# Optimization experiments

Measured on AMD Instinct MI355X. Metric: run time of the kernel, lower is better.

The kernel has to match this reference:

```python
import jax, jax.numpy as jnp
import numpy as np

B, S, HID, H = 8, 128, 256, 4
DH = HID // H
FF = 4 * HID


def setup_inputs() -> dict:
    key = jax.random.key(0)
    ks = jax.random.split(key, 16)
    n = lambda i, shape: jax.random.normal(ks[i], shape, dtype=jnp.float32) * 0.02
    z = lambda shape: jnp.zeros(shape, dtype=jnp.float32)
    return dict(
        x=jax.random.normal(ks[0], (B, S, HID), dtype=jnp.float32),
        attention_mask=jnp.zeros((B, 1, S, S), dtype=jnp.float32),
        Wq=n(1, (HID, HID)), bq=z((HID,)),
        Wk=n(2, (HID, HID)), bk=z((HID,)),
        Wv=n(3, (HID, HID)), bv=z((HID,)),
        order_w=n(4, (2 * DH,)), order_b=z(()),
        dist_w=n(5, (2 * DH,)), dist_b=z(()),
        scalar=jax.random.normal(ks[6], (1,), dtype=jnp.float32),
        AWq=n(7, (HID, HID)), Abq=z((HID,)),
        AWk=n(8, (HID, HID)), Abk=z((HID,)),
        Wd=n(9, (HID, HID)), bd=z((HID,)),
        g1=jnp.ones((HID,), jnp.float32), beta1=z((HID,)),
        W1=n(10, (HID, FF)), b1=z((FF,)),
        W2=n(11, (FF, HID)), b2=z((HID,)),
        g2=jnp.ones((HID,), jnp.float32), beta2=z((HID,)),
    )


def _ln(t, g, b, eps=1e-12):
    m = t.mean(-1, keepdims=True)
    v = ((t - m) ** 2).mean(-1, keepdims=True)
    return (t - m) / jnp.sqrt(v + eps) * g + b


def _heads(t):
    # [B,S,HID] -> [B,H,S,DH]
    return t.reshape(B, S, H, DH).transpose(0, 2, 1, 3)


def reference(x, attention_mask, Wq, bq, Wk, bk, Wv, bv, order_w, order_b,
              dist_w, dist_b, scalar, AWq, Abq, AWk, Abk, Wd, bd,
              g1, beta1, W1, b1, W2, b2, g2, beta2):
    inv = 1.0 / jnp.sqrt(jnp.float32(DH))
    q = x @ Wq + bq
    k = x @ Wk + bk
    v = x @ Wv + bv
    qh, kh, vh = _heads(q), _heads(k), _heads(v)
    scores = jnp.einsum('bhqd,bhkd->bhqk', qh, kh)  # [B,H,S,S]

    # order/distance affines on concat(q_i, k_j): Linear(2*DH,1) decomposes into
    # per-token projections summed via broadcast (same math, no [B,H,S,S,2*DH] tensor)
    pr_order = jax.nn.sigmoid((qh @ order_w[:DH])[..., :, None]
                              + (kh @ order_w[DH:])[..., None, :] + order_b)
    gd_order = jnp.triu(jnp.ones((S, S), jnp.float32), k=1)
    err_order = (jnp.log(pr_order + 1e-24) * gd_order
                 + jnp.log(1.0 - pr_order + 1e-24) * (1.0 - gd_order))

    idx = jnp.arange(S)
    gd_dist = jnp.log(jnp.abs(idx[None, :] - idx[:, None]).astype(jnp.float32) + 1.0)
    pr_dist = ((qh @ dist_w[:DH])[..., :, None]
               + (kh @ dist_w[DH:])[..., None, :] + dist_b)
    err_dist = -jnp.square(gd_dist - pr_dist) * jnp.square(scalar[0]) * 0.5

    rich_scores = scores + err_order + err_dist
    softm = lambda s: jax.nn.softmax(s * inv + attention_mask, axis=-1)
    rich_probs = softm(rich_scores)
    origin_probs = softm(scores)

    # rich/calibrated combine ('fixed'): softmax(origin + 0.5 * rich)
    combined = jax.nn.softmax(origin_probs + 0.5 * rich_probs, axis=-1)

    # two-level attack attention on transformed mixed q/k
    aq, ak = _heads(q @ AWq + Abq), _heads(k @ AWk + Abk)
    attack_probs = softm(jnp.einsum('bhqd,bhkd->bhqk', aq, ak))
    final_probs = jax.nn.softmax(combined + 0.5 * attack_probs, axis=-1)

    ctx = jnp.einsum('bhqk,bhkd->bhqd', final_probs, vh)
    ctx = ctx.transpose(0, 2, 1, 3).reshape(B, S, HID)
    h = _ln(ctx @ Wd + bd + x, g1, beta1)
    f = jax.nn.gelu(h @ W1 + b1, approximate=False) @ W2 + b2
    return _ln(f + h, g2, beta2)
```

## Files before the change

### kernel.cpp

```cpp
#include <hip/hip_runtime.h>
#include <hip/hip_bf16.h>
#include <math.h>

#define B_  8
#define S_  128
#define HID_ 256
#define H_  4
#define DH_ 64
#define FF_ 1024
#define M_  (B_ * S_)

typedef _Float16 half_t;
typedef __attribute__((ext_vector_type(8))) _Float16 half8;
typedef __attribute__((ext_vector_type(4))) float floatx4;

enum { EP_F32 = 0, EP_F16 = 1, EP_F16B = 2, EP_GELU = 3, EP_PROJ = 4 };

__device__ __forceinline__ floatx4 mfma16(half8 a, half8 b, floatx4 c) {
    return __builtin_amdgcn_mfma_f32_16x16x32_f16(a, b, c, 0, 0, 0);
}

__device__ __forceinline__ float wred_sum(float v) {
#pragma unroll
    for (int o = 32; o >= 1; o >>= 1) v += __shfl_xor(v, o, 64);
    return v;
}
__device__ __forceinline__ float block_sum_256(float v, float* s4, int tid) {
    v = wred_sum(v);
    __syncthreads();
    if ((tid & 63) == 0) s4[tid >> 6] = v;
    __syncthreads();
    return s4[0] + s4[1] + s4[2] + s4[3];
}
__device__ __forceinline__ float qred_sum(float v) {
#pragma unroll
    for (int o = 1; o < 16; o <<= 1) v += __shfl_xor(v, o, 64);
    return v;
}
__device__ __forceinline__ void sm8(float (&v)[8]) {
    float s = 0.f;
#pragma unroll
    for (int j = 0; j < 8; ++j) { v[j] = __expf(v[j]); s += v[j]; }
    s = qred_sum(s);
    float r = 1.f / s;
#pragma unroll
    for (int j = 0; j < 8; ++j) v[j] *= r;
}

template<int EPI>
__device__ __forceinline__ void mgemm(
    const half_t* __restrict__ A, int ldA,
    const half_t* __restrict__ Bt, int ldB,
    int kLen, int m0, int n0,
    const float* __restrict__ bias,
    float* __restrict__ Cf, half_t* __restrict__ Ch, int ldC,
    const float* __restrict__ pw1, const float* __restrict__ pw2,
    float* __restrict__ po1, float* __restrict__ po2, int hsel)
{
    __shared__ half8 Asf[2][4][64];
    __shared__ half8 Bsf[2][4][64];

    const int tid = threadIdx.x;
    const int w = tid >> 6, l = tid & 63;
    const int sr = tid >> 2;
    const int sq = tid & 3;
    const int sdst = (sr & 15) | (sq << 4);
    const int smt = sr >> 4;
    const half_t* Ap = A + (size_t)(m0 + sr) * ldA + sq * 8;
    const half_t* Bp = Bt + (size_t)(n0 + sr) * ldB + sq * 8;

    half8 ra, rb;
    auto fetch = [&](int t) {
        ra = *(const half8*)(Ap + t * 32);
        rb = *(const half8*)(Bp + t * 32);
    };
    auto commit = [&](int buf) {
        Asf[buf][smt][sdst] = ra;
        Bsf[buf][smt][sdst] = rb;
    };

    floatx4 zero = {0.f, 0.f, 0.f, 0.f};
    floatx4 acc[4] = {zero, zero, zero, zero};
    const int kt = kLen >> 5;

    fetch(0);
    commit(0);
    __syncthreads();
    for (int t = 0; t < kt; ++t) {
        const bool more = (t + 1 < kt);
        if (more) fetch(t + 1);
        const int buf = t & 1;
        half8 a = Asf[buf][w][l];
        acc[0] = mfma16(a, Bsf[buf][0][l], acc[0]);
        acc[1] = mfma16(a, Bsf[buf][1][l], acc[1]);
        acc[2] = mfma16(a, Bsf[buf][2][l], acc[2]);
        acc[3] = mfma16(a, Bsf[buf][3][l], acc[3]);
        if (more) {
            commit((t + 1) & 1);
            __syncthreads();
        }
    }

    const int quad = l >> 4, lc = l & 15;
    const int rowb = m0 + w * 16 + quad * 4;
    float bvv[4] = {0.f, 0.f, 0.f, 0.f};
    if (EPI >= EP_F16B) {
#pragma unroll
        for (int nt = 0; nt < 4; ++nt) bvv[nt] = bias[n0 + nt * 16 + lc];
    }
    float pw1v[4], pw2v[4];
    if (EPI == EP_PROJ) {
#pragma unroll
        for (int nt = 0; nt < 4; ++nt) {
            pw1v[nt] = pw1[nt * 16 + lc];
            pw2v[nt] = pw2[nt * 16 + lc];
        }
    }
#pragma unroll
    for (int rr = 0; rr < 4; ++rr) {
        float ov[4];
#pragma unroll
        for (int nt = 0; nt < 4; ++nt) {
            float o = acc[nt][rr];
            if (EPI >= EP_F16B) o += bvv[nt];
            if (EPI == EP_GELU) o = 0.5f * o * (1.f + erff(o * 0.70710678118654752f));
            ov[nt] = o;
            const size_t ci = (size_t)(rowb + rr) * ldC + n0 + nt * 16 + lc;
            if (EPI == EP_F32) Cf[ci] = o;
            else Ch[ci] = (half_t)o;
        }
        if (EPI == EP_PROJ) {
            float po = ov[0] * pw1v[0] + ov[1] * pw1v[1] + ov[2] * pw1v[2] + ov[3] * pw1v[3];
            float pd = ov[0] * pw2v[0] + ov[1] * pw2v[1] + ov[2] * pw2v[2] + ov[3] * pw2v[3];
#pragma unroll
            for (int off = 1; off < 16; off <<= 1) {
                po += __shfl_xor(po, off, 64);
                pd += __shfl_xor(pd, off, 64);
            }
            if (lc == 0) {
                const int m = rowb + rr;
                const int idx = ((m >> 7) * H_ + hsel) * S_ + (m & 127);
                po1[idx] = po;
                po2[idx] = pd;
            }
        }
    }
}

__global__ __launch_bounds__(256) void prep_kernel(
    const float* __restrict__ x,
    const float* __restrict__ Wq, const float* __restrict__ Wk,
    const float* __restrict__ Wv, const float* __restrict__ Wd,
    const float* __restrict__ AWq, const float* __restrict__ AWk,
    const float* __restrict__ W1, const float* __restrict__ W2,
    half_t* __restrict__ x16, half_t* __restrict__ Wq16n, half_t* __restrict__ Wk16n,
    half_t* __restrict__ WqT, half_t* __restrict__ WkT, half_t* __restrict__ WvT,
    half_t* __restrict__ WdT, half_t* __restrict__ AWqT, half_t* __restrict__ AWkT,
    half_t* __restrict__ W1T, half_t* __restrict__ W2T)
{
    const int z = blockIdx.z, bx = blockIdx.x, by = blockIdx.y;
    const int tid = threadIdx.x;
    if (z < 3) {
        const float* src = (z == 0) ? x : (z == 1) ? Wq : Wk;
        half_t* dst = (z == 0) ? x16 : (z == 1) ? Wq16n : Wk16n;
        const int total = (z == 0) ? M_ * HID_ : HID_ * HID_;
        const int bid = by * 16 + bx;
        if (bid * 1024 < total) {
            const int base = bid * 1024 + tid * 4;
            float4 vv = *(const float4*)(src + base);
            dst[base + 0] = (half_t)vv.x;
            dst[base + 1] = (half_t)vv.y;
            dst[base + 2] = (half_t)vv.z;
            dst[base + 3] = (half_t)vv.w;
        }
        return;
    }
    const float* src; half_t* dst; int K, N, k0, n0;
    if (z <= 8) {
        const float* ins[6] = {Wq, Wk, Wv, Wd, AWq, AWk};
        half_t* outs[6] = {WqT, WkT, WvT, WdT, AWqT, AWkT};
        src = ins[z - 3]; dst = outs[z - 3];
        K = 256; N = 256; k0 = bx * 64; n0 = by * 64;
        if (bx >= 4 || by >= 4) return;
    } else if (z == 9) {
        src = W1; dst = W1T; K = 256; N = 1024;
        k0 = bx * 64; n0 = by * 64;
        if (bx >= 4) return;
    } else {
        src = W2; dst = W2T; K = 1024; N = 256;
        k0 = by * 64; n0 = bx * 64;
        if (bx >= 4) return;
    }
    __shared__ half_t tl[64][72];
    const int r = tid >> 2, c0 = (tid & 3) * 16;
#pragma unroll 4
    for (int i = 0; i < 16; ++i)
        tl[c0 + i][r] = (half_t)src[(size_t)(k0 + r) * N + n0 + c0 + i];
    __syncthreads();
#pragma unroll 4
    for (int i = 0; i < 16; ++i)
        dst[(size_t)(n0 + r) * K + k0 + c0 + i] = tl[r][c0 + i];
}

__global__ __launch_bounds__(256) void compose_mfma(
    const half_t* __restrict__ AWqT, const half_t* __restrict__ AWkT,
    const half_t* __restrict__ Wq16n, const half_t* __restrict__ Wk16n,
    const float* __restrict__ AWq, const float* __restrict__ AWk,
    const float* __restrict__ bq, const float* __restrict__ bk,
    const float* __restrict__ Abq, const float* __restrict__ Abk,
    half_t* __restrict__ WcqT, half_t* __restrict__ WckT,
    float* __restrict__ bcq, float* __restrict__ bck)
{
    const int z = blockIdx.z;
    if (blockIdx.y < 4) {
        const half_t* A = z ? AWkT : AWqT;
        const half_t* Bt = z ? Wk16n : Wq16n;
        half_t* C = z ? WckT : WcqT;
        mgemm<EP_F16>(A, HID_, Bt, HID_, HID_, blockIdx.y * 64, blockIdx.x * 64,
                      nullptr, nullptr, C, HID_, nullptr, nullptr, nullptr, nullptr, 0);
    } else {
        __shared__ float red[4][64];
        const float* bsrc = z ? bk : bq;
        const float* AW   = z ? AWk : AWq;
        const float* Ab   = z ? Abk : Abq;
        float* bco        = z ? bck : bcq;
        int t = threadIdx.x, l = t & 63, kc = t >> 6;
        int n = blockIdx.x * 64 + l;
        float p = 0.f;
#pragma unroll 8
        for (int kk = 0; kk < 64; ++kk) {
            int k = kc * 64 + kk;
            p = fmaf(bsrc[k], AW[(size_t)k * HID_ + n], p);
        }
        red[kc][l] = p;
        __syncthreads();
        if (kc == 0)
            bco[n] = red[0][l] + red[1][l] + red[2][l] + red[3][l] + Ab[n];
    }
}

__global__ __launch_bounds__(256) void xgemm5(
    const half_t* __restrict__ x16,
    const half_t* __restrict__ WqT, const float* __restrict__ bq,
    const half_t* __restrict__ WkT, const float* __restrict__ bk,
    const half_t* __restrict__ WvT, const float* __restrict__ bv,
    const half_t* __restrict__ WcqT, const float* __restrict__ bcq,
    const half_t* __restrict__ WckT, const float* __restrict__ bck,
    const float* __restrict__ order_w, const float* __restrict__ dist_w,
    half_t* __restrict__ q16, half_t* __restrict__ k16, half_t* __restrict__ v16,
    half_t* __restrict__ aq16, half_t* __restrict__ ak16,
    float* __restrict__ qoA, float* __restrict__ qdA,
    float* __restrict__ koA, float* __restrict__ kdA)
{
    const int z = blockIdx.z;
    const int m0 = blockIdx.y * 64, n0 = blockIdx.x * 64;
    if (z == 0)
        mgemm<EP_PROJ>(x16, HID_, WqT, HID_, HID_, m0, n0, bq, nullptr, q16, HID_,
                       order_w, dist_w, qoA, qdA, blockIdx.x);
    else if (z == 1)
        mgemm<EP_PROJ>(x16, HID_, WkT, HID_, HID_, m0, n0, bk, nullptr, k16, HID_,
                       order_w + DH_, dist_w + DH_, koA, kdA, blockIdx.x);
    else if (z == 2)
        mgemm<EP_F16B>(x16, HID_, WvT, HID_, HID_, m0, n0, bv, nullptr, v16, HID_,
                       nullptr, nullptr, nullptr, nullptr, 0);
    else if (z == 3)
        mgemm<EP_F16B>(x16, HID_, WcqT, HID_, HID_, m0, n0, bcq, nullptr, aq16, HID_,
                       nullptr, nullptr, nullptr, nullptr, 0);
    else
        mgemm<EP_F16B>(x16, HID_, WckT, HID_, HID_, m0, n0, bck, nullptr, ak16, HID_,
                       nullptr, nullptr, nullptr, nullptr, 0);
}

__global__ __launch_bounds__(64) void attn_fused(
    const half_t* __restrict__ q16, const half_t* __restrict__ k16,
    const half_t* __restrict__ v16, const half_t* __restrict__ aq16,
    const half_t* __restrict__ ak16,
    const float* __restrict__ qoA, const float* __restrict__ qdA,
    const float* __restrict__ koA, const float* __restrict__ kdA,
    const float* __restrict__ mask,
    const float* __restrict__ order_b_p, const float* __restrict__ dist_b_p,
    const float* __restrict__ scalar_p,
    half_t* __restrict__ ctx16)
{
    __shared__ half8 Qf[2][64], AQf[2][64];
    __shared__ half8 Kf[2][8][64], AKf[2][8][64];
    __shared__ half_t Vt[64][136];
    __shared__ half_t Pm[16][136];

    const int l = threadIdx.x;
    const int quad = l >> 4, lc = l & 15;
    const int bh = blockIdx.x >> 3, rt = blockIdx.x & 7;
    const int b = bh >> 2, h = bh & 3;
    const size_t hoff = (size_t)b * S_ * HID_ + h * DH_;

#pragma unroll
    for (int u = 0; u < 2; ++u) {
        int idx = u * 64 + l;
        int r = idx >> 3, c = idx & 7;
        size_t g = hoff + (size_t)(rt * 16 + r) * HID_ + c * 8;
        int kt = c >> 2, sl = r | ((c & 3) << 4);
        Qf[kt][sl]  = *(const half8*)(q16 + g);
        AQf[kt][sl] = *(const half8*)(aq16 + g);
    }
#pragma unroll
    for (int u = 0; u < 16; ++u) {
        int idx = u * 64 + l;
        int j = idx >> 3, c = idx & 7;
        size_t g = hoff + (size_t)j * HID_ + c * 8;
        int kt = c >> 2, jt = j >> 4, sl = (j & 15) | ((c & 3) << 4);
        Kf[kt][jt][sl]  = *(const half8*)(k16 + g);
        AKf[kt][jt][sl] = *(const half8*)(ak16 + g);
    }
#pragma unroll
    for (int u = 0; u < 16; ++u) {
        int j = (u >> 3) * 64 + l;
        int c = u & 7;
        half8 vv = *(const half8*)(v16 + hoff + (size_t)j * HID_ + c * 8);
#pragma unroll
        for (int e = 0; e < 8; ++e) Vt[c * 8 + e][j] = vv[e];
    }
    __syncthreads();

    floatx4 zero = {0.f, 0.f, 0.f, 0.f};
    floatx4 accS[8], accA[8];
#pragma unroll
    for (int jt = 0; jt < 8; ++jt) { accS[jt] = zero; accA[jt] = zero; }
#pragma unroll
    for (int kt = 0; kt < 2; ++kt) {
        half8 a0 = Qf[kt][l];
        half8 a1 = AQf[kt][l];
#pragma unroll
        for (int jt = 0; jt < 8; ++jt) {
            accS[jt] = mfma16(a0, Kf[kt][jt][l], accS[jt]);
            accA[jt] = mfma16(a1, AKf[kt][jt][l], accA[jt]);
        }
    }

    const float ob = order_b_p[0], db = dist_b_p[0];
    const float scl = scalar_p[0];
    const float s2 = scl * scl;
    const float inv = 0.125f;
    float kov[8], kdv[8];
#pragma unroll
    for (int jt = 0; jt < 8; ++jt) {
        kov[jt] = koA[bh * S_ + jt * 16 + lc];
        kdv[jt] = kdA[bh * S_ + jt * 16 + lc];
    }
#pragma unroll
    for (int reg = 0; reg < 4; ++reg) {
        const int il = quad * 4 + reg;
        const int i  = rt * 16 + il;
        float qo = qoA[bh * S_ + i], qd = qdA[bh * S_ + i];
        const float* mrow = mask + ((size_t)(b * S_ + i)) * S_;
        float mk[8], lg[8], as_[8];
#pragma unroll
        for (int jt = 0; jt < 8; ++jt) {
            mk[jt] = mrow[jt * 16 + lc];
            lg[jt] = accS[jt][reg];
            as_[jt] = accA[jt][reg];
        }
        float p0[8];
#pragma unroll
        for (int jt = 0; jt < 8; ++jt) p0[jt] = lg[jt] * inv + mk[jt];
        sm8(p0);
        float p1[8];
#pragma unroll
        for (int jt = 0; jt < 8; ++jt) {
            int j = jt * 16 + lc;
            float pr = 1.f / (1.f + __expf(-(qo + kov[jt] + ob)));
            float sel = (j > i) ? pr : 1.f - pr;
            float erro = __logf(sel + 1e-24f);
            float gd = __logf(fabsf((float)(j - i)) + 1.f);
            float dd = gd - (qd + kdv[jt] + db);
            p1[jt] = (lg[jt] + erro - 0.5f * dd * dd * s2) * inv + mk[jt];
        }
        sm8(p1);
#pragma unroll
        for (int jt = 0; jt < 8; ++jt) p0[jt] += 0.5f * p1[jt];
        sm8(p0);
#pragma unroll
        for (int jt = 0; jt < 8; ++jt) p1[jt] = as_[jt] * inv + mk[jt];
        sm8(p1);
#pragma unroll
        for (int jt = 0; jt < 8; ++jt) p0[jt] += 0.5f * p1[jt];
        sm8(p0);
#pragma unroll
        for (int jt = 0; jt < 8; ++jt) Pm[il][jt * 16 + lc] = (half_t)p0[jt];
    }
    __syncthreads();

    half8 pa_[4];
#pragma unroll
    for (int kt = 0; kt < 4; ++kt)
        pa_[kt] = *(const half8*)&Pm[lc][kt * 32 + quad * 8];
    floatx4 apv[4];
#pragma unroll
    for (int nt = 0; nt < 4; ++nt) apv[nt] = zero;
#pragma unroll
    for (int nt = 0; nt < 4; ++nt) {
#pragma unroll
        for (int kt = 0; kt < 4; ++kt) {
            half8 vf = *(const half8*)&Vt[nt * 16 + lc][kt * 32 + quad * 8];
            apv[nt] = mfma16(pa_[kt], vf, apv[nt]);
        }
    }
#pragma unroll
    for (int nt = 0; nt < 4; ++nt) {
#pragma unroll
        for (int reg = 0; reg < 4; ++reg) {
            int i = rt * 16 + quad * 4 + reg;
            ctx16[hoff + (size_t)i * HID_ + nt * 16 + lc] = (half_t)apv[nt][reg];
        }
    }
}

__global__ __launch_bounds__(256) void gemmln(
    const half_t* __restrict__ A, const half_t* __restrict__ Bt,
    const float* __restrict__ bias, const float* __restrict__ res,
    const float* __restrict__ g, const float* __restrict__ be,
    float* __restrict__ out32, half_t* __restrict__ out16)
{
    __shared__ half8 Asf[2][64];
    __shared__ half8 Bsf[2][16][64];
    __shared__ float rsum[4][16], rsq[4][16];

    const int tid = threadIdx.x;
    const int w = tid >> 6, l = tid & 63;
    const int quad = l >> 4, lc = l & 15;
    const int m0 = blockIdx.x * 16;
    const int K = HID_;

    const int ar = tid >> 2, akq = tid & 3;
    const half_t* Ap = A + (size_t)(m0 + ar) * K + akq * 8;
    const half_t* Bp = Bt + (size_t)tid * K;

    half8 ra, rb[4];
    auto fetch = [&](int t) {
        if (tid < 64) ra = *(const half8*)(Ap + t * 32);
        const half_t* bp = Bp + t * 32;
#pragma unroll
        for (int u = 0; u < 4; ++u) rb[u] = *(const half8*)(bp + u * 8);
    };
    auto commit = [&](int buf) {
        if (tid < 64) Asf[buf][ar | (akq << 4)] = ra;
#pragma unroll
        for (int u = 0; u < 4; ++u)
            Bsf[buf][tid >> 4][(tid & 15) | (u << 4)] = rb[u];
    };

    floatx4 zero = {0.f, 0.f, 0.f, 0.f};
    floatx4 acc[4] = {zero, zero, zero, zero};
    const int ktiles = K >> 5;

    fetch(0);
    commit(0);
    __syncthreads();
    for (int t = 0; t < ktiles; ++t) {
        const bool more = (t + 1 < ktiles);
        if (more) fetch(t + 1);
        const int buf = t & 1;
        half8 a = Asf[buf][l];
#pragma unroll
        for (int nt = 0; nt < 4; ++nt)
            acc[nt] = mfma16(a, Bsf[buf][w * 4 + nt][l], acc[nt]);
        if (more) {
            commit((t + 1) & 1);
            __syncthreads();
        }
    }

    float bv[4], gg[4], bb[4];
#pragma unroll
    for (int nt = 0; nt < 4; ++nt) {
        const int col = w * 64 + nt * 16 + lc;
        bv[nt] = bias[col];
        gg[nt] = g[col];
        bb[nt] = be[col];
    }
    float vals[4][4];
#pragma unroll
    for (int reg = 0; reg < 4; ++reg) {
        const int rl = quad * 4 + reg;
        const float* rr = res + (size_t)(m0 + rl) * HID_;
        float s = 0.f, sq = 0.f;
#pragma unroll
        for (int nt = 0; nt < 4; ++nt) {
            float vvv = acc[nt][reg] + bv[nt] + rr[w * 64 + nt * 16 + lc];
            vals[reg][nt] = vvv;
            s += vvv;
            sq += vvv * vvv;
        }
        s = qred_sum(s);
        sq = qred_sum(sq);
        if (lc == 0) { rsum[w][rl] = s; rsq[w][rl] = sq; }
    }
    __syncthreads();
#pragma unroll
    for (int reg = 0; reg < 4; ++reg) {
        const int rl = quad * 4 + reg;
        float tot = rsum[0][rl] + rsum[1][rl] + rsum[2][rl] + rsum[3][rl];
        float tsq = rsq[0][rl] + rsq[1][rl] + rsq[2][rl] + rsq[3][rl];
        float mean = tot * (1.f / HID_);
        float var = tsq * (1.f / HID_) - mean * mean;
        float rstd = rsqrtf(var + 1e-12f);
#pragma unroll
        for (int nt = 0; nt < 4; ++nt) {
            float o = (vals[reg][nt] - mean) * rstd * gg[nt] + bb[nt];
            const size_t ci = (size_t)(m0 + rl) * HID_ + w * 64 + nt * 16 + lc;
            out32[ci] = o;
            out16[ci] = (half_t)o;
        }
    }
}

__global__ __launch_bounds__(256) void ff1_mfma(
    const half_t* __restrict__ h16, const half_t* __restrict__ W1T,
    const float* __restrict__ b1, half_t* __restrict__ f116)
{
    mgemm<EP_GELU>(h16, HID_, W1T, HID_, HID_, blockIdx.y * 64, blockIdx.x * 64,
                   b1, nullptr, f116, FF_, nullptr, nullptr, nullptr, nullptr, 0);
}

__global__ __launch_bounds__(256) void ff2_mfma(
    const half_t* __restrict__ f116, const half_t* __restrict__ W2T,
    float* __restrict__ p0, float* __restrict__ p1,
    float* __restrict__ p2, float* __restrict__ p3)
{
    const int z = blockIdx.z;
    float* C = (z == 0) ? p0 : (z == 1) ? p1 : (z == 2) ? p2 : p3;
    mgemm<EP_F32>(f116 + z * 256, FF_, W2T + z * 256, FF_, 256,
                  blockIdx.y * 64, blockIdx.x * 64,
                  nullptr, C, nullptr, HID_, nullptr, nullptr, nullptr, nullptr, 0);
}

__global__ __launch_bounds__(256) void ln2_kernel(
    const float* __restrict__ p0, const float* __restrict__ p1,
    const float* __restrict__ p2, const float* __restrict__ p3,
    const float* __restrict__ b2, const float* __restrict__ h32,
    const float* __restrict__ g2, const float* __restrict__ beta2,
    float* __restrict__ out)
{
    __shared__ float s4[4];
    const int row = blockIdx.x;
    const int n = threadIdx.x;
    const size_t idx = (size_t)row * HID_ + n;
    float val = p0[idx] + p1[idx] + p2[idx] + p3[idx] + b2[n] + h32[idx];
    float mean = block_sum_256(val, s4, n) * (1.f / HID_);
    float dv = val - mean;
    float var = block_sum_256(dv * dv, s4, n) * (1.f / HID_);
    out[idx] = dv * rsqrtf(var + 1e-12f) * g2[n] + beta2[n];
}

extern "C" void kernel_launch(void* const* d_in, const int* in_sizes, int n_in,
                              void* d_out, int out_size, void* d_ws, size_t ws_size,
                              hipStream_t stream) {
    const float* x        = (const float*)d_in[0];
    const float* mask     = (const float*)d_in[1];
    const float* Wq       = (const float*)d_in[2];
    const float* bq       = (const float*)d_in[3];
    const float* Wk       = (const float*)d_in[4];
    const float* bk       = (const float*)d_in[5];
    const float* Wv       = (const float*)d_in[6];
    const float* bv       = (const float*)d_in[7];
    const float* order_w  = (const float*)d_in[8];
    const float* order_b  = (const float*)d_in[9];
    const float* dist_w   = (const float*)d_in[10];
    const float* dist_b   = (const float*)d_in[11];
    const float* scalar   = (const float*)d_in[12];
    const float* AWq      = (const float*)d_in[13];
    const float* Abq      = (const float*)d_in[14];
    const float* AWk      = (const float*)d_in[15];
    const float* Abk      = (const float*)d_in[16];
    const float* Wd       = (const float*)d_in[17];
    const float* bd       = (const float*)d_in[18];
    const float* g1       = (const float*)d_in[19];
    const float* beta1    = (const float*)d_in[20];
    const float* W1       = (const float*)d_in[21];
    const float* b1       = (const float*)d_in[22];
    const float* W2       = (const float*)d_in[23];
    const float* b2       = (const float*)d_in[24];
    const float* g2       = (const float*)d_in[25];
    const float* beta2    = (const float*)d_in[26];

    float* ws = (float*)d_ws;
    size_t off = 0;
    auto afl = [&](size_t n) { float* p = ws + off; off += n; return p; };
    auto ahf = [&](size_t nh) { half_t* p = (half_t*)(ws + off); off += nh / 2; return p; };

    half_t* x16   = ahf(M_ * HID_);
    half_t* Wq16n = ahf(HID_ * HID_);
    half_t* Wk16n = ahf(HID_ * HID_);
    half_t* WqT   = ahf(HID_ * HID_);
    half_t* WkT   = ahf(HID_ * HID_);
    half_t* WvT   = ahf(HID_ * HID_);
    half_t* WdT   = ahf(HID_ * HID_);
    half_t* AWqT  = ahf(HID_ * HID_);
    half_t* AWkT  = ahf(HID_ * HID_);
    half_t* W1T   = ahf(HID_ * FF_);
    half_t* W2T   = ahf(HID_ * FF_);
    half_t* WcqT  = ahf(HID_ * HID_);
    half_t* WckT  = ahf(HID_ * HID_);
    half_t* q16   = ahf(M_ * HID_);
    half_t* k16   = ahf(M_ * HID_);
    half_t* v16   = ahf(M_ * HID_);
    half_t* aq16  = ahf(M_ * HID_);
    half_t* ak16  = ahf(M_ * HID_);
    half_t* ctx16 = ahf(M_ * HID_);
    half_t* h16   = ahf(M_ * HID_);
    half_t* f116  = ahf(M_ * FF_);
    float* hb32 = afl(M_ * HID_);
    float* pf0  = afl(M_ * HID_);
    float* pf1  = afl(M_ * HID_);
    float* pf2  = afl(M_ * HID_);
    float* pf3  = afl(M_ * HID_);
    float* bcq  = afl(256);
    float* bck  = afl(256);
    float* qoA  = afl(B_ * H_ * S_);
    float* qdA  = afl(B_ * H_ * S_);
    float* koA  = afl(B_ * H_ * S_);
    float* kdA  = afl(B_ * H_ * S_);

    prep_kernel<<<dim3(16, 16, 11), 256, 0, stream>>>(
        x, Wq, Wk, Wv, Wd, AWq, AWk, W1, W2,
        x16, Wq16n, Wk16n, WqT, WkT, WvT, WdT, AWqT, AWkT, W1T, W2T);
    compose_mfma<<<dim3(4, 5, 2), 256, 0, stream>>>(
        AWqT, AWkT, Wq16n, Wk16n, AWq, AWk, bq, bk, Abq, Abk, WcqT, WckT, bcq, bck);
    xgemm5<<<dim3(4, 16, 5), 256, 0, stream>>>(
        x16, WqT, bq, WkT, bk, WvT, bv, WcqT, bcq, WckT, bck, order_w, dist_w,
        q16, k16, v16, aq16, ak16, qoA, qdA, koA, kdA);
    attn_fused<<<256, 64, 0, stream>>>(
        q16, k16, v16, aq16, ak16, qoA, qdA, koA, kdA,
        mask, order_b, dist_b, scalar, ctx16);
    gemmln<<<64, 256, 0, stream>>>(ctx16, WdT, bd, x, g1, beta1, hb32, h16);
    ff1_mfma<<<dim3(16, 16), 256, 0, stream>>>(h16, W1T, b1, f116);
    ff2_mfma<<<dim3(4, 16, 4), 256, 0, stream>>>(f116, W2T, pf0, pf1, pf2, pf3);
    ln2_kernel<<<M_, 256, 0, stream>>>(pf0, pf1, pf2, pf3, b2, hb32, g2, beta2, (float*)d_out);
}
```

Before: 168.9 us.

## Fuse FF2 GEMM with final LayerNorm and emit V pre-transposed

The split-K FF2 GEMM and its separate LayerNorm kernel become one templated gemmln pass with K=1024, so the four fp32 partial buffers are no longer written and re-read and one launch is dropped. The V projection epilogue now writes V already transposed per head, which replaces the scalar scatter into shared memory inside attention with vector half8 copies. The cost is that FF2 now runs on only 64 blocks with a long K loop, so far less parallelism than the 256-block split-K version.

```diff
diff --git a/kernel.cpp b/kernel.cpp
--- a/kernel.cpp
+++ b/kernel.cpp
@@ -11,10 +11,11 @@
 #define M_  (B_ * S_)
 
 typedef _Float16 half_t;
+typedef __attribute__((ext_vector_type(4))) _Float16 half4;
 typedef __attribute__((ext_vector_type(8))) _Float16 half8;
 typedef __attribute__((ext_vector_type(4))) float floatx4;
 
-enum { EP_F32 = 0, EP_F16 = 1, EP_F16B = 2, EP_GELU = 3, EP_PROJ = 4 };
+enum { EP_F32 = 0, EP_F16 = 1, EP_F16B = 2, EP_GELU = 3, EP_PROJ = 4, EP_VT = 5 };
 
 __device__ __forceinline__ floatx4 mfma16(half8 a, half8 b, floatx4 c) {
     return __builtin_amdgcn_mfma_f32_16x16x32_f16(a, b, c, 0, 0, 0);
@@ -24,13 +25,6 @@
 #pragma unroll
     for (int o = 32; o >= 1; o >>= 1) v += __shfl_xor(v, o, 64);
     return v;
-}
-__device__ __forceinline__ float block_sum_256(float v, float* s4, int tid) {
-    v = wred_sum(v);
-    __syncthreads();
-    if ((tid & 63) == 0) s4[tid >> 6] = v;
-    __syncthreads();
-    return s4[0] + s4[1] + s4[2] + s4[3];
 }
 __device__ __forceinline__ float qred_sum(float v) {
 #pragma unroll
@@ -107,6 +101,20 @@
     if (EPI >= EP_F16B) {
 #pragma unroll
         for (int nt = 0; nt < 4; ++nt) bvv[nt] = bias[n0 + nt * 16 + lc];
+    }
+    if (EPI == EP_VT) {
+        const int b = rowb >> 7;
+        const int jb = rowb & 127;
+        const int h = n0 >> 6;
+#pragma unroll
+        for (int nt = 0; nt < 4; ++nt) {
+            const int d = nt * 16 + lc;
+            half4 v4;
+#pragma unroll
+            for (int rr = 0; rr < 4; ++rr) v4[rr] = (half_t)(acc[nt][rr] + bvv[nt]);
+            *(half4*)(Ch + (((size_t)b * H_ + h) * 64 + d) * 128 + jb) = v4;
+        }
+        return;
     }
     float pw1v[4], pw2v[4];
     if (EPI == EP_PROJ) {
@@ -247,7 +255,7 @@
     const half_t* __restrict__ WcqT, const float* __restrict__ bcq,
     const half_t* __restrict__ WckT, const float* __restrict__ bck,
     const float* __restrict__ order_w, const float* __restrict__ dist_w,
-    half_t* __restrict__ q16, half_t* __restrict__ k16, half_t* __restrict__ v16,
+    half_t* __restrict__ q16, half_t* __restrict__ k16, half_t* __restrict__ vt16,
     half_t* __restrict__ aq16, half_t* __restrict__ ak16,
     float* __restrict__ qoA, float* __restrict__ qdA,
     float* __restrict__ koA, float* __restrict__ kdA)
@@ -261,8 +269,8 @@
         mgemm<EP_PROJ>(x16, HID_, WkT, HID_, HID_, m0, n0, bk, nullptr, k16, HID_,
                        order_w + DH_, dist_w + DH_, koA, kdA, blockIdx.x);
     else if (z == 2)
-        mgemm<EP_F16B>(x16, HID_, WvT, HID_, HID_, m0, n0, bv, nullptr, v16, HID_,
-                       nullptr, nullptr, nullptr, nullptr, 0);
+        mgemm<EP_VT>(x16, HID_, WvT, HID_, HID_, m0, n0, bv, nullptr, vt16, HID_,
+                     nullptr, nullptr, nullptr, nullptr, 0);
     else if (z == 3)
         mgemm<EP_F16B>(x16, HID_, WcqT, HID_, HID_, m0, n0, bcq, nullptr, aq16, HID_,
                        nullptr, nullptr, nullptr, nullptr, 0);
@@ -273,7 +281,7 @@
 
 __global__ __launch_bounds__(64) void attn_fused(
     const half_t* __restrict__ q16, const half_t* __restrict__ k16,
-    const half_t* __restrict__ v16, const half_t* __restrict__ aq16,
+    const half_t* __restrict__ vt16, const half_t* __restrict__ aq16,
     const half_t* __restrict__ ak16,
     const float* __restrict__ qoA, const float* __restrict__ qdA,
     const float* __restrict__ koA, const float* __restrict__ kdA,
@@ -313,11 +321,10 @@
     }
 #pragma unroll
     for (int u = 0; u < 16; ++u) {
-        int j = (u >> 3) * 64 + l;
-        int c = u & 7;
-        half8 vv = *(const half8*)(v16 + hoff + (size_t)j * HID_ + c * 8);
-#pragma unroll
-        for (int e = 0; e < 8; ++e) Vt[c * 8 + e][j] = vv[e];
+        int idx = u * 64 + l;
+        int d = idx >> 4, jc = idx & 15;
+        half8 vv = *(const half8*)(vt16 + ((size_t)bh * 64 + d) * 128 + jc * 8);
+        *(half8*)&Vt[d][jc * 8] = vv;
     }
     __syncthreads();
 
@@ -414,8 +421,9 @@
     }
 }
 
+template<int WRITE16>
 __global__ __launch_bounds__(256) void gemmln(
-    const half_t* __restrict__ A, const half_t* __restrict__ Bt,
+    const half_t* __restrict__ A, const half_t* __restrict__ Bt, int K,
     const float* __restrict__ bias, const float* __restrict__ res,
     const float* __restrict__ g, const float* __restrict__ be,
     float* __restrict__ out32, half_t* __restrict__ out16)
@@ -428,24 +436,25 @@
     const int w = tid >> 6, l = tid & 63;
     const int quad = l >> 4, lc = l & 15;
     const int m0 = blockIdx.x * 16;
-    const int K = HID_;
-
-    const int ar = tid >> 2, akq = tid & 3;
-    const half_t* Ap = A + (size_t)(m0 + ar) * K + akq * 8;
-    const half_t* Bp = Bt + (size_t)tid * K;
+
+    const int sr = tid >> 2, skq = tid & 3;
+    const half_t* Ap = A + (size_t)(m0 + (sr & 15)) * K + skq * 8;
+    const half_t* Bp = Bt + (size_t)sr * K + skq * 8;
 
     half8 ra, rb[4];
     auto fetch = [&](int t) {
         if (tid < 64) ra = *(const half8*)(Ap + t * 32);
-        const half_t* bp = Bp + t * 32;
-#pragma unroll
-        for (int u = 0; u < 4; ++u) rb[u] = *(const half8*)(bp + u * 8);
+#pragma unroll
+        for (int u = 0; u < 4; ++u)
+            rb[u] = *(const half8*)(Bp + (size_t)(u * 64) * K + t * 32);
     };
     auto commit = [&](int buf) {
-        if (tid < 64) Asf[buf][ar | (akq << 4)] = ra;
-#pragma unroll
-        for (int u = 0; u < 4; ++u)
-            Bsf[buf][tid >> 4][(tid & 15) | (u << 4)] = rb[u];
+        if (tid < 64) Asf[buf][(sr & 15) | (skq << 4)] = ra;
+#pragma unroll
+        for (int u = 0; u < 4; ++u) {
+            const int row = sr + u * 64;
+            Bsf[buf][row >> 4][(row & 15) | (skq << 4)] = rb[u];
+        }
     };
 
     floatx4 zero = {0.f, 0.f, 0.f, 0.f};
@@ -508,7 +517,7 @@
             float o = (vals[reg][nt] - mean) * rstd * gg[nt] + bb[nt];
             const size_t ci = (size_t)(m0 + rl) * HID_ + w * 64 + nt * 16 + lc;
             out32[ci] = o;
-            out16[ci] = (half_t)o;
+            if (WRITE16) out16[ci] = (half_t)o;
         }
     }
 }
@@ -519,36 +528,6 @@
 {
     mgemm<EP_GELU>(h16, HID_, W1T, HID_, HID_, blockIdx.y * 64, blockIdx.x * 64,
                    b1, nullptr, f116, FF_, nullptr, nullptr, nullptr, nullptr, 0);
-}
-
-__global__ __launch_bounds__(256) void ff2_mfma(
-    const half_t* __restrict__ f116, const half_t* __restrict__ W2T,
-    float* __restrict__ p0, float* __restrict__ p1,
-    float* __restrict__ p2, float* __restrict__ p3)
-{
-    const int z = blockIdx.z;
-    float* C = (z == 0) ? p0 : (z == 1) ? p1 : (z == 2) ? p2 : p3;
-    mgemm<EP_F32>(f116 + z * 256, FF_, W2T + z * 256, FF_, 256,
-                  blockIdx.y * 64, blockIdx.x * 64,
-                  nullptr, C, nullptr, HID_, nullptr, nullptr, nullptr, nullptr, 0);
-}
-
-__global__ __launch_bounds__(256) void ln2_kernel(
-    const float* __restrict__ p0, const float* __restrict__ p1,
-    const float* __restrict__ p2, const float* __restrict__ p3,
-    const float* __restrict__ b2, const float* __restrict__ h32,
-    const float* __restrict__ g2, const float* __restrict__ beta2,
-    float* __restrict__ out)
-{
-    __shared__ float s4[4];
-    const int row = blockIdx.x;
-    const int n = threadIdx.x;
-    const size_t idx = (size_t)row * HID_ + n;
-    float val = p0[idx] + p1[idx] + p2[idx] + p3[idx] + b2[n] + h32[idx];
-    float mean = block_sum_256(val, s4, n) * (1.f / HID_);
-    float dv = val - mean;
-    float var = block_sum_256(dv * dv, s4, n) * (1.f / HID_);
-    out[idx] = dv * rsqrtf(var + 1e-12f) * g2[n] + beta2[n];
 }
 
 extern "C" void kernel_launch(void* const* d_in, const int* in_sizes, int n_in,
@@ -602,17 +581,13 @@
     half_t* WckT  = ahf(HID_ * HID_);
     half_t* q16   = ahf(M_ * HID_);
     half_t* k16   = ahf(M_ * HID_);
-    half_t* v16   = ahf(M_ * HID_);
+    half_t* vt16  = ahf(M_ * HID_);
     half_t* aq16  = ahf(M_ * HID_);
     half_t* ak16  = ahf(M_ * HID_);
     half_t* ctx16 = ahf(M_ * HID_);
     half_t* h16   = ahf(M_ * HID_);
     half_t* f116  = ahf(M_ * FF_);
     float* hb32 = afl(M_ * HID_);
-    float* pf0  = afl(M_ * HID_);
-    float* pf1  = afl(M_ * HID_);
-    float* pf2  = afl(M_ * HID_);
-    float* pf3  = afl(M_ * HID_);
     float* bcq  = afl(256);
     float* bck  = afl(256);
     float* qoA  = afl(B_ * H_ * S_);
@@ -627,12 +602,12 @@
         AWqT, AWkT, Wq16n, Wk16n, AWq, AWk, bq, bk, Abq, Abk, WcqT, WckT, bcq, bck);
     xgemm5<<<dim3(4, 16, 5), 256, 0, stream>>>(
         x16, WqT, bq, WkT, bk, WvT, bv, WcqT, bcq, WckT, bck, order_w, dist_w,
-        q16, k16, v16, aq16, ak16, qoA, qdA, koA, kdA);
+        q16, k16, vt16, aq16, ak16, qoA, qdA, koA, kdA);
     attn_fused<<<256, 64, 0, stream>>>(
-        q16, k16, v16, aq16, ak16, qoA, qdA, koA, kdA,
+        q16, k16, vt16, aq16, ak16, qoA, qdA, koA, kdA,
         mask, order_b, dist_b, scalar, ctx16);
-    gemmln<<<64, 256, 0, stream>>>(ctx16, WdT, bd, x, g1, beta1, hb32, h16);
+    gemmln<1><<<64, 256, 0, stream>>>(ctx16, WdT, HID_, bd, x, g1, beta1, hb32, h16);
     ff1_mfma<<<dim3(16, 16), 256, 0, stream>>>(h16, W1T, b1, f116);
-    ff2_mfma<<<dim3(4, 16, 4), 256, 0, stream>>>(f116, W2T, pf0, pf1, pf2, pf3);
-    ln2_kernel<<<M_, 256, 0, stream>>>(pf0, pf1, pf2, pf3, b2, hb32, g2, beta2, (float*)d_out);
-}
+    gemmln<0><<<64, 256, 0, stream>>>(f116, W2T, FF_, b2, hb32, g2, beta2,
+                                      (float*)d_out, nullptr);
+}
```

After: 184.7 us. 1.09x slower.
